# Optimization experiments

Measured on AMD Instinct MI355X. Metric: run time of the kernel, lower is better.

## Reference

```python
import math
import jax, jax.numpy as jnp
import numpy as np

N, E, H, D, NNZ = 32768, 512, 8, 64, 524288


def setup_inputs() -> dict:
    key = jax.random.key(0)
    ks = jax.random.split(key, 12)
    x = jax.random.normal(ks[0], (N, E), dtype=jnp.float32)
    row_index = jnp.sort(jax.random.randint(ks[1], (NNZ,), 0, N))
    col_index = jax.random.randint(ks[2], (NNZ,), 0, N)
    to_col_index = jax.random.randint(ks[3], (N,), 0, N)
    att_bias = jax.random.normal(ks[4], (H, NNZ), dtype=jnp.float32)
    # positive interatomic distances in ~[0.5, 5.5)
    dist = jax.random.uniform(ks[5], (NNZ,), dtype=jnp.float32) * 5.0 + 0.5
    pos = jax.random.normal(ks[6], (N, 3), dtype=jnp.float32)
    col_pos = jax.random.normal(ks[7], (N, 3), dtype=jnp.float32)
    s = 1.0 / math.sqrt(E)
    q_w = jax.random.normal(ks[8], (E, E), dtype=jnp.float32) * s
    q_b = jax.random.normal(ks[9], (E,), dtype=jnp.float32) * 0.02
    k_w = jax.random.normal(ks[10], (E, E), dtype=jnp.float32) * s
    k_b = jax.random.normal(ks[11], (E,), dtype=jnp.float32) * 0.02
    return {"x": x, "row_index": row_index, "col_index": col_index,
            "to_col_index": to_col_index, "att_bias": att_bias, "dist": dist,
            "pos": pos, "col_pos": col_pos,
            "q_w": q_w, "q_b": q_b, "k_w": k_w, "k_b": k_b}


def reference(x, row_index, col_index, to_col_index, att_bias, dist, pos, col_pos,
              q_w, q_b, k_w, k_b):
    n = x.shape[0]
    h = att_bias.shape[0]
    d = x.shape[1] // h
    # per-head projections: [N, H, D]
    q = (x @ q_w.T + q_b).reshape(n, h, d) * (1.0 / math.sqrt(d))
    k = (x @ k_w.T + k_b).reshape(n, h, d)[to_col_index]  # [Nk, H, D]
    # sparse (COO) masked q @ k^T plus additive bias -> per-edge logits [nnz, H]
    logits = jnp.einsum('ehd,ehd->eh', q[row_index], k[col_index]) + att_bias.T
    # sparse softmax over each query row (per head)
    m = jax.ops.segment_max(logits, row_index, num_segments=n)       # [N, H]
    p = jnp.exp(logits - m[row_index])
    z = jax.ops.segment_sum(p, row_index, num_segments=n)            # [N, H]
    att = p / z[row_index]                                           # [nnz, H]
    # distance-weighted attention (dist==0 -> contribution 0, as x/inf in torch)
    inv_d = jnp.where(dist == 0, 0.0, 1.0 / dist)
    att = att * inv_d[:, None]
    # sparse bmm against col_pos values and against ones
    cp = col_pos[col_index]                                          # [nnz, 3]
    dst_vec = jax.ops.segment_sum(att[:, :, None] * cp[:, None, :],
                                  row_index, num_segments=n)         # [N, H, 3]
    avg_inv_dist = jax.ops.segment_sum(att, row_index, num_segments=n)  # [N, H]
    src_vec = avg_inv_dist[..., None] * pos[:, None, :]              # [N, H, 3]
    v = dst_vec - src_vec
    norm = jnp.sqrt(jnp.sum(v * v, axis=-1, keepdims=True))
    feat3 = v / jnp.maximum(norm, 1e-12)                             # F.normalize
    feat = jnp.concatenate([feat3, avg_inv_dist[..., None]], axis=-1)  # [N, H, 4]
    return feat.reshape(n, h * 4)
```

## Files before the change

kernel.cpp:

```cpp
#include <hip/hip_runtime.h>
#include <math.h>
#include <stdint.h>

#define N_NODES 32768
#define E_DIM   512
#define H_HEADS 8
#define D_HEAD  64
#define NNZ_E   524288

typedef __attribute__((ext_vector_type(4))) float f32x4;
typedef __attribute__((ext_vector_type(8))) short bf16x8;
typedef __attribute__((ext_vector_type(8))) short s16x8;

__device__ __forceinline__ unsigned short f32_to_bf16_rne(float f) {
  union { float f; uint32_t u; } v; v.f = f;
  const uint32_t u = v.u;
  return (unsigned short)((u + 0x7FFFu + ((u >> 16) & 1u)) >> 16);
}
__device__ __forceinline__ float bf16_to_f32(unsigned short h) {
  union { uint32_t u; float f; } v; v.u = ((uint32_t)h) << 16;
  return v.f;
}

__device__ __forceinline__ void async16(const void* g, void* l) {
  __builtin_amdgcn_global_load_lds(
      (const __attribute__((address_space(1))) void*)g,
      (__attribute__((address_space(3))) void*)l, 16, 0, 0);
}

__global__ __launch_bounds__(256) void prep_small(
    const float* __restrict__ x,
    const float* __restrict__ q_w, const float* __restrict__ k_w,
    const int* __restrict__ row_index, const int* __restrict__ col_index,
    const int* __restrict__ to_col,
    unsigned short* __restrict__ wq_s, unsigned short* __restrict__ wk_s,
    unsigned short* __restrict__ xs,
    int* __restrict__ row_start, int* __restrict__ ge) {
  const int b = blockIdx.x;
  if (b < 512 + 16384) {
    const float* src;
    unsigned short* dst;
    int t;
    if (b < 256)      { src = q_w; dst = wq_s; t = b * 256 + threadIdx.x; }
    else if (b < 512) { src = k_w; dst = wk_s; t = (b - 256) * 256 + threadIdx.x; }
    else              { src = x;   dst = xs;   t = (b - 512) * 256 + threadIdx.x; }
    const int r = t >> 7;
    const int c4 = (t & 127) << 2;
    const float4 v = *(const float4*)(src + (size_t)r * 512 + c4);
    ushort4 hi, lo;
    hi.x = f32_to_bf16_rne(v.x); lo.x = f32_to_bf16_rne(v.x - bf16_to_f32(hi.x));
    hi.y = f32_to_bf16_rne(v.y); lo.y = f32_to_bf16_rne(v.y - bf16_to_f32(hi.y));
    hi.z = f32_to_bf16_rne(v.z); lo.z = f32_to_bf16_rne(v.z - bf16_to_f32(hi.z));
    hi.w = f32_to_bf16_rne(v.w); lo.w = f32_to_bf16_rne(v.w - bf16_to_f32(hi.w));
    *(ushort4*)(dst + (size_t)r * 1024 + c4) = hi;
    *(ushort4*)(dst + (size_t)r * 1024 + 512 + c4) = lo;
  } else {
    const int e = (b - 512 - 16384) * 256 + threadIdx.x;
    if (e < NNZ_E) {
      ge[e] = to_col[col_index[e]];
      const int r0 = row_index[e];
      const int r1 = (e + 1 < NNZ_E) ? row_index[e + 1] : N_NODES;
      if (e == 0)
        for (int r = 0; r <= r0; ++r) row_start[r] = 0;
      for (int r = r0 + 1; r <= r1; ++r) row_start[r] = e + 1;
    }
  }
}

__global__ __launch_bounds__(256) void gemm_mfma(
    const unsigned short* __restrict__ xs,
    const unsigned short* __restrict__ wqs,
    const unsigned short* __restrict__ wks,
    const float* __restrict__ q_b, const float* __restrict__ k_b,
    short* __restrict__ q16, short* __restrict__ k16) {
  __shared__ unsigned short Ah[128 * 32];
  __shared__ unsigned short Al[128 * 32];
  __shared__ unsigned short Bh[128 * 32];
  __shared__ unsigned short Bl[128 * 32];
  const int tid = threadIdx.x;
  const int w = tid >> 6;
  const int l = tid & 63;

  const int b = blockIdx.x;
  const int j = b >> 3;
  const int mb = (b & 7) * 32 + (j >> 3);
  const int c = j & 7;
  const bool is_q = ((c & 1) == 0);
  const int bm = mb * 128;
  const int bn = (c >> 1) * 128;

  const unsigned short* __restrict__ wmat = is_q ? wqs : wks;
  const float* __restrict__ bias = is_q ? q_b : k_b;
  short* __restrict__ outp = is_q ? q16 : k16;
  const float oscale = is_q ? 2048.f : 4096.f;

  const int wm = (w & 1) * 64;
  const int wn = (w >> 1) * 64;

  f32x4 acc[4][4];
#pragma unroll
  for (int i = 0; i < 4; ++i)
#pragma unroll
    for (int jj = 0; jj < 4; ++jj) acc[i][jj] = (f32x4){0.f, 0.f, 0.f, 0.f};

  const int sr0 = w * 16 + (l >> 2);
  const int sr1 = sr0 + 64;
  const int sc = (((l & 3) ^ ((l >> 3) & 3)) << 3);
  const int fr = l & 15;
  const int fcs = ((((l >> 4) ^ ((fr >> 1) & 3)) & 3) << 3);

  const unsigned short* __restrict__ wa = wmat + (size_t)bn * 1024;
  const unsigned short* __restrict__ xa = xs + (size_t)bm * 1024;

  for (int k0 = 0; k0 < 512; k0 += 32) {
    async16(xa + (size_t)sr0 * 1024 + k0 + sc, Ah + w * 512);
    async16(xa + (size_t)sr1 * 1024 + k0 + sc, Ah + (w + 4) * 512);
    async16(xa + (size_t)sr0 * 1024 + 512 + k0 + sc, Al + w * 512);
    async16(xa + (size_t)sr1 * 1024 + 512 + k0 + sc, Al + (w + 4) * 512);
    async16(wa + (size_t)sr0 * 1024 + k0 + sc, Bh + w * 512);
    async16(wa + (size_t)sr1 * 1024 + k0 + sc, Bh + (w + 4) * 512);
    async16(wa + (size_t)sr0 * 1024 + 512 + k0 + sc, Bl + w * 512);
    async16(wa + (size_t)sr1 * 1024 + 512 + k0 + sc, Bl + (w + 4) * 512);
    __syncthreads();

    bf16x8 ahi[4], alo[4], bh[4];
#pragma unroll
    for (int i = 0; i < 4; ++i)
      ahi[i] = *(const bf16x8*)(Ah + (wm + i * 16 + fr) * 32 + fcs);
#pragma unroll
    for (int i = 0; i < 4; ++i)
      alo[i] = *(const bf16x8*)(Al + (wm + i * 16 + fr) * 32 + fcs);
#pragma unroll
    for (int i = 0; i < 4; ++i)
      bh[i] = *(const bf16x8*)(Bh + (wn + i * 16 + fr) * 32 + fcs);
#pragma unroll
    for (int i = 0; i < 4; ++i)
#pragma unroll
      for (int jj = 0; jj < 4; ++jj)
        acc[i][jj] = __builtin_amdgcn_mfma_f32_16x16x32_bf16(
            ahi[i], bh[jj], acc[i][jj], 0, 0, 0);
#pragma unroll
    for (int i = 0; i < 4; ++i)
#pragma unroll
      for (int jj = 0; jj < 4; ++jj)
        acc[i][jj] = __builtin_amdgcn_mfma_f32_16x16x32_bf16(
            alo[i], bh[jj], acc[i][jj], 0, 0, 0);
#pragma unroll
    for (int jj = 0; jj < 4; ++jj)
      bh[jj] = *(const bf16x8*)(Bl + (wn + jj * 16 + fr) * 32 + fcs);
#pragma unroll
    for (int i = 0; i < 4; ++i)
#pragma unroll
      for (int jj = 0; jj < 4; ++jj)
        acc[i][jj] = __builtin_amdgcn_mfma_f32_16x16x32_bf16(
            ahi[i], bh[jj], acc[i][jj], 0, 0, 0);
    __syncthreads();
  }

  const int cn = l & 15;
  const int cm4 = (l >> 4) * 4;
  float bvals[4];
#pragma unroll
  for (int jj = 0; jj < 4; ++jj) bvals[jj] = bias[bn + wn + jj * 16 + cn];
#pragma unroll
  for (int i = 0; i < 4; ++i) {
#pragma unroll
    for (int r = 0; r < 4; ++r) {
      const int m = bm + wm + i * 16 + cm4 + r;
      short* op = outp + (size_t)m * 512 + bn + wn + cn;
#pragma unroll
      for (int jj = 0; jj < 4; ++jj) {
        float v = (acc[i][jj][r] + bvals[jj]) * oscale;
        v = fmaxf(fminf(v, 32767.f), -32767.f);
        op[jj * 16] = (short)__float2int_rn(v);
      }
    }
  }
}

__global__ __launch_bounds__(256) void row_fused(
    const short* __restrict__ q16, const short* __restrict__ k16,
    const int* __restrict__ row_start, const int* __restrict__ ge,
    const float* __restrict__ att_bias, const int* __restrict__ col_index,
    const float* __restrict__ dist, const float* __restrict__ pos,
    const float* __restrict__ col_pos, float* __restrict__ out) {
  const int r = blockIdx.x * 4 + (threadIdx.x >> 6);
  const int lane = threadIdx.x & 63;
  const int h = lane >> 3;
  const int start = row_start[r];
  const int end = row_start[r + 1];

  const s16x8 qv = *(const s16x8*)(q16 + (size_t)r * E_DIM + lane * 8);
  const float* __restrict__ biasp = att_bias + (size_t)h * NNZ_E;

  float m = -INFINITY, l = 0.f, accw = 0.f, a0 = 0.f, a1 = 0.f, a2 = 0.f;

  auto dotk = [&](const s16x8 kv) -> float {
    float s = (float)qv[0] * (float)kv[0];
    s = fmaf((float)qv[1], (float)kv[1], s);
    s = fmaf((float)qv[2], (float)kv[2], s);
    s = fmaf((float)qv[3], (float)kv[3], s);
    s = fmaf((float)qv[4], (float)kv[4], s);
    s = fmaf((float)qv[5], (float)kv[5], s);
    s = fmaf((float)qv[6], (float)kv[6], s);
    s = fmaf((float)qv[7], (float)kv[7], s);
    s += __shfl_xor(s, 1);
    s += __shfl_xor(s, 2);
    s += __shfl_xor(s, 4);
    return s;
  };
  auto upd = [&](float logit, float dd, float c0, float c1, float c2) {
    const float w = (dd == 0.f) ? 0.f : 1.f / dd;
    const float nm = fmaxf(m, logit);
    const float sc = __expf(m - nm);
    const float p = __expf(logit - nm);
    m = nm;
    l = fmaf(l, sc, p);
    const float pw = p * w;
    accw = fmaf(accw, sc, pw);
    a0 = fmaf(a0, sc, pw * c0);
    a1 = fmaf(a1, sc, pw * c1);
    a2 = fmaf(a2, sc, pw * c2);
  };

  int e = start;
  for (; e + 2 <= end; e += 2) {
    const int g0 = ge[e], g1 = ge[e + 1];
    const s16x8 kv0 = *(const s16x8*)(k16 + (size_t)g0 * E_DIM + lane * 8);
    const s16x8 kv1 = *(const s16x8*)(k16 + (size_t)g1 * E_DIM + lane * 8);
    const int c0 = col_index[e], c1 = col_index[e + 1];
    const float dd0 = dist[e], dd1 = dist[e + 1];
    const float bb0 = biasp[e], bb1 = biasp[e + 1];
    const float cp00 = col_pos[c0 * 3 + 0];
    const float cp01 = col_pos[c0 * 3 + 1];
    const float cp02 = col_pos[c0 * 3 + 2];
    const float cp10 = col_pos[c1 * 3 + 0];
    const float cp11 = col_pos[c1 * 3 + 1];
    const float cp12 = col_pos[c1 * 3 + 2];
    const float s0 = dotk(kv0) * (1.f / 67108864.f) + bb0;
    const float s1 = dotk(kv1) * (1.f / 67108864.f) + bb1;
    upd(s0, dd0, cp00, cp01, cp02);
    upd(s1, dd1, cp10, cp11, cp12);
  }
  if (e < end) {
    const int g0 = ge[e];
    const s16x8 kv0 = *(const s16x8*)(k16 + (size_t)g0 * E_DIM + lane * 8);
    const int c0 = col_index[e];
    const float dd0 = dist[e];
    const float bb0 = biasp[e];
    const float cp00 = col_pos[c0 * 3 + 0];
    const float cp01 = col_pos[c0 * 3 + 1];
    const float cp02 = col_pos[c0 * 3 + 2];
    const float s0 = dotk(kv0) * (1.f / 67108864.f) + bb0;
    upd(s0, dd0, cp00, cp01, cp02);
  }

  if ((lane & 7) == 0) {
    const float invz = (l > 0.f) ? 1.f / l : 0.f;
    const float avg = accw * invz;
    const float v0 = a0 * invz - avg * pos[r * 3 + 0];
    const float v1 = a1 * invz - avg * pos[r * 3 + 1];
    const float v2 = a2 * invz - avg * pos[r * 3 + 2];
    const float nrm = sqrtf(v0 * v0 + v1 * v1 + v2 * v2);
    const float invn = 1.f / fmaxf(nrm, 1e-12f);
    float4 o;
    o.x = v0 * invn; o.y = v1 * invn; o.z = v2 * invn; o.w = avg;
    *(float4*)(out + (size_t)r * (H_HEADS * 4) + h * 4) = o;
  }
}

extern "C" void kernel_launch(void* const* d_in, const int* in_sizes, int n_in,
                              void* d_out, int out_size, void* d_ws,
                              size_t ws_size, hipStream_t stream) {
  const float* x        = (const float*)d_in[0];
  const int* row_index  = (const int*)d_in[1];
  const int* col_index  = (const int*)d_in[2];
  const int* to_col     = (const int*)d_in[3];
  const float* att_bias = (const float*)d_in[4];
  const float* dist     = (const float*)d_in[5];
  const float* pos      = (const float*)d_in[6];
  const float* col_pos  = (const float*)d_in[7];
  const float* q_w      = (const float*)d_in[8];
  const float* q_b      = (const float*)d_in[9];
  const float* k_w      = (const float*)d_in[10];
  const float* k_b      = (const float*)d_in[11];
  float* out = (float*)d_out;

  short* q16 = (short*)d_ws;
  short* k16 = q16 + (size_t)N_NODES * E_DIM;
  unsigned short* xs = (unsigned short*)(k16 + (size_t)N_NODES * E_DIM);
  unsigned short* wq_s = xs + (size_t)N_NODES * 1024;
  unsigned short* wk_s = wq_s + 512 * 1024;
  int* row_start = (int*)(wk_s + 512 * 1024);
  int* ge = row_start + (N_NODES + 1);

  prep_small<<<512 + 16384 + NNZ_E / 256, 256, 0, stream>>>(
      x, q_w, k_w, row_index, col_index, to_col, wq_s, wk_s, xs, row_start, ge);

  gemm_mfma<<<2048, 256, 0, stream>>>(xs, wq_s, wk_s, q_b, k_b, q16, k16);

  row_fused<<<N_NODES / 4, 256, 0, stream>>>(q16, k16, row_start, ge, att_bias,
                                             col_index, dist, pos, col_pos,
                                             out);
}
```

Before: 320.4 us.

## Replace split-bf16 GEMM with single fp16 MFMA and unroll edge loop by four

The projection GEMM previously split x and the weights into hi/lo bf16 pairs and ran three MFMA passes to approach fp32 accuracy. It now converts the inputs once to fp16 and runs a single f16 MFMA pass, which halves the converted-operand storage and staging traffic and cuts the matrix work to a third. The per-row attention loop is also unrolled from two to four edges so more gathered k loads are in flight at once. The cost is lower precision in q and k (fp16 mantissa, no compensation term), and fp16 range could overflow on large inputs.

```diff
diff --git a/kernel.cpp b/kernel.cpp
--- a/kernel.cpp
+++ b/kernel.cpp
@@ -9,18 +9,8 @@
 #define NNZ_E   524288
 
 typedef __attribute__((ext_vector_type(4))) float f32x4;
-typedef __attribute__((ext_vector_type(8))) short bf16x8;
+typedef __attribute__((ext_vector_type(8))) _Float16 f16x8;
 typedef __attribute__((ext_vector_type(8))) short s16x8;
-
-__device__ __forceinline__ unsigned short f32_to_bf16_rne(float f) {
-  union { float f; uint32_t u; } v; v.f = f;
-  const uint32_t u = v.u;
-  return (unsigned short)((u + 0x7FFFu + ((u >> 16) & 1u)) >> 16);
-}
-__device__ __forceinline__ float bf16_to_f32(unsigned short h) {
-  union { uint32_t u; float f; } v; v.u = ((uint32_t)h) << 16;
-  return v.f;
-}
 
 __device__ __forceinline__ void async16(const void* g, void* l) {
   __builtin_amdgcn_global_load_lds(
@@ -33,29 +23,29 @@
     const float* __restrict__ q_w, const float* __restrict__ k_w,
     const int* __restrict__ row_index, const int* __restrict__ col_index,
     const int* __restrict__ to_col,
-    unsigned short* __restrict__ wq_s, unsigned short* __restrict__ wk_s,
-    unsigned short* __restrict__ xs,
+    _Float16* __restrict__ wq_h, _Float16* __restrict__ wk_h,
+    _Float16* __restrict__ xs,
     int* __restrict__ row_start, int* __restrict__ ge) {
   const int b = blockIdx.x;
-  if (b < 512 + 16384) {
+  if (b < 8448) {
     const float* src;
-    unsigned short* dst;
+    _Float16* dst;
     int t;
-    if (b < 256)      { src = q_w; dst = wq_s; t = b * 256 + threadIdx.x; }
-    else if (b < 512) { src = k_w; dst = wk_s; t = (b - 256) * 256 + threadIdx.x; }
-    else              { src = x;   dst = xs;   t = (b - 512) * 256 + threadIdx.x; }
-    const int r = t >> 7;
-    const int c4 = (t & 127) << 2;
-    const float4 v = *(const float4*)(src + (size_t)r * 512 + c4);
-    ushort4 hi, lo;
-    hi.x = f32_to_bf16_rne(v.x); lo.x = f32_to_bf16_rne(v.x - bf16_to_f32(hi.x));
-    hi.y = f32_to_bf16_rne(v.y); lo.y = f32_to_bf16_rne(v.y - bf16_to_f32(hi.y));
-    hi.z = f32_to_bf16_rne(v.z); lo.z = f32_to_bf16_rne(v.z - bf16_to_f32(hi.z));
-    hi.w = f32_to_bf16_rne(v.w); lo.w = f32_to_bf16_rne(v.w - bf16_to_f32(hi.w));
-    *(ushort4*)(dst + (size_t)r * 1024 + c4) = hi;
-    *(ushort4*)(dst + (size_t)r * 1024 + 512 + c4) = lo;
+    if (b < 128)      { src = q_w; dst = wq_h; t = b * 256 + threadIdx.x; }
+    else if (b < 256) { src = k_w; dst = wk_h; t = (b - 128) * 256 + threadIdx.x; }
+    else              { src = x;   dst = xs;   t = (b - 256) * 256 + threadIdx.x; }
+    const int r = t >> 6;
+    const int c8 = (t & 63) << 3;
+    const float4 v0 = *(const float4*)(src + (size_t)r * 512 + c8);
+    const float4 v1 = *(const float4*)(src + (size_t)r * 512 + c8 + 4);
+    f16x8 o;
+    o[0] = (_Float16)v0.x; o[1] = (_Float16)v0.y;
+    o[2] = (_Float16)v0.z; o[3] = (_Float16)v0.w;
+    o[4] = (_Float16)v1.x; o[5] = (_Float16)v1.y;
+    o[6] = (_Float16)v1.z; o[7] = (_Float16)v1.w;
+    *(f16x8*)(dst + (size_t)r * 512 + c8) = o;
   } else {
-    const int e = (b - 512 - 16384) * 256 + threadIdx.x;
+    const int e = (b - 8448) * 256 + threadIdx.x;
     if (e < NNZ_E) {
       ge[e] = to_col[col_index[e]];
       const int r0 = row_index[e];
@@ -68,15 +58,13 @@
 }
 
 __global__ __launch_bounds__(256) void gemm_mfma(
-    const unsigned short* __restrict__ xs,
-    const unsigned short* __restrict__ wqs,
-    const unsigned short* __restrict__ wks,
+    const _Float16* __restrict__ xs,
+    const _Float16* __restrict__ wqh,
+    const _Float16* __restrict__ wkh,
     const float* __restrict__ q_b, const float* __restrict__ k_b,
     short* __restrict__ q16, short* __restrict__ k16) {
-  __shared__ unsigned short Ah[128 * 32];
-  __shared__ unsigned short Al[128 * 32];
-  __shared__ unsigned short Bh[128 * 32];
-  __shared__ unsigned short Bl[128 * 32];
+  __shared__ _Float16 Ah[128 * 32];
+  __shared__ _Float16 Bh[128 * 32];
   const int tid = threadIdx.x;
   const int w = tid >> 6;
   const int l = tid & 63;
@@ -89,7 +77,7 @@
   const int bm = mb * 128;
   const int bn = (c >> 1) * 128;
 
-  const unsigned short* __restrict__ wmat = is_q ? wqs : wks;
+  const _Float16* __restrict__ wmat = is_q ? wqh : wkh;
   const float* __restrict__ bias = is_q ? q_b : k_b;
   short* __restrict__ outp = is_q ? q16 : k16;
   const float oscale = is_q ? 2048.f : 4096.f;
@@ -109,51 +97,29 @@
   const int fr = l & 15;
   const int fcs = ((((l >> 4) ^ ((fr >> 1) & 3)) & 3) << 3);
 
-  const unsigned short* __restrict__ wa = wmat + (size_t)bn * 1024;
-  const unsigned short* __restrict__ xa = xs + (size_t)bm * 1024;
+  const _Float16* __restrict__ wa = wmat + (size_t)bn * 512;
+  const _Float16* __restrict__ xa = xs + (size_t)bm * 512;
 
   for (int k0 = 0; k0 < 512; k0 += 32) {
-    async16(xa + (size_t)sr0 * 1024 + k0 + sc, Ah + w * 512);
-    async16(xa + (size_t)sr1 * 1024 + k0 + sc, Ah + (w + 4) * 512);
-    async16(xa + (size_t)sr0 * 1024 + 512 + k0 + sc, Al + w * 512);
-    async16(xa + (size_t)sr1 * 1024 + 512 + k0 + sc, Al + (w + 4) * 512);
-    async16(wa + (size_t)sr0 * 1024 + k0 + sc, Bh + w * 512);
-    async16(wa + (size_t)sr1 * 1024 + k0 + sc, Bh + (w + 4) * 512);
-    async16(wa + (size_t)sr0 * 1024 + 512 + k0 + sc, Bl + w * 512);
-    async16(wa + (size_t)sr1 * 1024 + 512 + k0 + sc, Bl + (w + 4) * 512);
+    async16(xa + (size_t)sr0 * 512 + k0 + sc, Ah + w * 512);
+    async16(xa + (size_t)sr1 * 512 + k0 + sc, Ah + (w + 4) * 512);
+    async16(wa + (size_t)sr0 * 512 + k0 + sc, Bh + w * 512);
+    async16(wa + (size_t)sr1 * 512 + k0 + sc, Bh + (w + 4) * 512);
     __syncthreads();
 
-    bf16x8 ahi[4], alo[4], bh[4];
-#pragma unroll
-    for (int i = 0; i < 4; ++i)
-      ahi[i] = *(const bf16x8*)(Ah + (wm + i * 16 + fr) * 32 + fcs);
-#pragma unroll
-    for (int i = 0; i < 4; ++i)
-      alo[i] = *(const bf16x8*)(Al + (wm + i * 16 + fr) * 32 + fcs);
-#pragma unroll
-    for (int i = 0; i < 4; ++i)
-      bh[i] = *(const bf16x8*)(Bh + (wn + i * 16 + fr) * 32 + fcs);
+    f16x8 av[4], bv[4];
+#pragma unroll
+    for (int i = 0; i < 4; ++i)
+      av[i] = *(const f16x8*)(Ah + (wm + i * 16 + fr) * 32 + fcs);
+#pragma unroll
+    for (int i = 0; i < 4; ++i)
+      bv[i] = *(const f16x8*)(Bh + (wn + i * 16 + fr) * 32 + fcs);
 #pragma unroll
     for (int i = 0; i < 4; ++i)
 #pragma unroll
       for (int jj = 0; jj < 4; ++jj)
-        acc[i][jj] = __builtin_amdgcn_mfma_f32_16x16x32_bf16(
-            ahi[i], bh[jj], acc[i][jj], 0, 0, 0);
-#pragma unroll
-    for (int i = 0; i < 4; ++i)
-#pragma unroll
-      for (int jj = 0; jj < 4; ++jj)
-        acc[i][jj] = __builtin_amdgcn_mfma_f32_16x16x32_bf16(
-            alo[i], bh[jj], acc[i][jj], 0, 0, 0);
-#pragma unroll
-    for (int jj = 0; jj < 4; ++jj)
-      bh[jj] = *(const bf16x8*)(Bl + (wn + jj * 16 + fr) * 32 + fcs);
-#pragma unroll
-    for (int i = 0; i < 4; ++i)
-#pragma unroll
-      for (int jj = 0; jj < 4; ++jj)
-        acc[i][jj] = __builtin_amdgcn_mfma_f32_16x16x32_bf16(
-            ahi[i], bh[jj], acc[i][jj], 0, 0, 0);
+        acc[i][jj] = __builtin_amdgcn_mfma_f32_16x16x32_f16(
+            av[i], bv[jj], acc[i][jj], 0, 0, 0);
     __syncthreads();
   }
 
@@ -224,25 +190,35 @@
   };
 
   int e = start;
-  for (; e + 2 <= end; e += 2) {
-    const int g0 = ge[e], g1 = ge[e + 1];
-    const s16x8 kv0 = *(const s16x8*)(k16 + (size_t)g0 * E_DIM + lane * 8);
-    const s16x8 kv1 = *(const s16x8*)(k16 + (size_t)g1 * E_DIM + lane * 8);
-    const int c0 = col_index[e], c1 = col_index[e + 1];
-    const float dd0 = dist[e], dd1 = dist[e + 1];
-    const float bb0 = biasp[e], bb1 = biasp[e + 1];
-    const float cp00 = col_pos[c0 * 3 + 0];
-    const float cp01 = col_pos[c0 * 3 + 1];
-    const float cp02 = col_pos[c0 * 3 + 2];
-    const float cp10 = col_pos[c1 * 3 + 0];
-    const float cp11 = col_pos[c1 * 3 + 1];
-    const float cp12 = col_pos[c1 * 3 + 2];
-    const float s0 = dotk(kv0) * (1.f / 67108864.f) + bb0;
-    const float s1 = dotk(kv1) * (1.f / 67108864.f) + bb1;
-    upd(s0, dd0, cp00, cp01, cp02);
-    upd(s1, dd1, cp10, cp11, cp12);
-  }
-  if (e < end) {
+  for (; e + 4 <= end; e += 4) {
+    int g[4], cc[4];
+    float dd[4], bb[4], cp[4][3];
+    s16x8 kv[4];
+#pragma unroll
+    for (int i = 0; i < 4; ++i) g[i] = ge[e + i];
+#pragma unroll
+    for (int i = 0; i < 4; ++i)
+      kv[i] = *(const s16x8*)(k16 + (size_t)g[i] * E_DIM + lane * 8);
+#pragma unroll
+    for (int i = 0; i < 4; ++i) {
+      cc[i] = col_index[e + i];
+      dd[i] = dist[e + i];
+      bb[i] = biasp[e + i];
+    }
+#pragma unroll
+    for (int i = 0; i < 4; ++i) {
+      cp[i][0] = col_pos[cc[i] * 3 + 0];
+      cp[i][1] = col_pos[cc[i] * 3 + 1];
+      cp[i][2] = col_pos[cc[i] * 3 + 2];
+    }
+    float s[4];
+#pragma unroll
+    for (int i = 0; i < 4; ++i)
+      s[i] = dotk(kv[i]) * (1.f / 67108864.f) + bb[i];
+#pragma unroll
+    for (int i = 0; i < 4; ++i) upd(s[i], dd[i], cp[i][0], cp[i][1], cp[i][2]);
+  }
+  for (; e < end; ++e) {
     const int g0 = ge[e];
     const s16x8 kv0 = *(const s16x8*)(k16 + (size_t)g0 * E_DIM + lane * 8);
     const int c0 = col_index[e];
@@ -288,16 +264,16 @@
 
   short* q16 = (short*)d_ws;
   short* k16 = q16 + (size_t)N_NODES * E_DIM;
-  unsigned short* xs = (unsigned short*)(k16 + (size_t)N_NODES * E_DIM);
-  unsigned short* wq_s = xs + (size_t)N_NODES * 1024;
-  unsigned short* wk_s = wq_s + 512 * 1024;
-  int* row_start = (int*)(wk_s + 512 * 1024);
+  _Float16* xs = (_Float16*)(k16 + (size_t)N_NODES * E_DIM);
+  _Float16* wq_h = xs + (size_t)N_NODES * 512;
+  _Float16* wk_h = wq_h + 512 * 512;
+  int* row_start = (int*)(wk_h + 512 * 512);
   int* ge = row_start + (N_NODES + 1);
 
-  prep_small<<<512 + 16384 + NNZ_E / 256, 256, 0, stream>>>(
-      x, q_w, k_w, row_index, col_index, to_col, wq_s, wk_s, xs, row_start, ge);
-
-  gemm_mfma<<<2048, 256, 0, stream>>>(xs, wq_s, wk_s, q_b, k_b, q16, k16);
+  prep_small<<<8448 + NNZ_E / 256, 256, 0, stream>>>(
+      x, q_w, k_w, row_index, col_index, to_col, wq_h, wk_h, xs, row_start, ge);
+
+  gemm_mfma<<<2048, 256, 0, stream>>>(xs, wq_h, wk_h, q_b, k_b, q16, k16);
 
   row_fused<<<N_NODES / 4, 256, 0, stream>>>(q16, k16, row_start, ge, att_bias,
                                              col_index, dist, pos, col_pos,
```

New measurement: 261.6 us. 18.4% less time.
